# Optimization experiments

Hardware: AMD Instinct MI355X
Metric: run time of the kernel (lower is better)

The kernel has to match this reference:

```python
import jax, jax.numpy as jnp
import numpy as np

D_MODEL = 1024
D_CODEX = 64
CODEX_SIZE = 8192
BETA = 1.0
EPS_NORM = 1e-12
EPS_LN = 1e-5


def l2norm(x):
    # F.normalize(p=2, dim=-1, eps=1e-12): x / max(||x||, eps)
    n = jnp.sqrt(jnp.sum(x * x, axis=-1, keepdims=True))
    return x / jnp.maximum(n, EPS_NORM)


def setup_inputs() -> dict:
    key = jax.random.key(0)
    ks = jax.random.split(key, 8)
    B, S = 4, 2048
    Z = jax.random.normal(ks[0], (B, S, D_MODEL), dtype=jnp.float32)
    W1 = 0.02 * jax.random.normal(ks[1], (D_MODEL, D_MODEL), dtype=jnp.float32)
    b1 = jnp.zeros((D_MODEL,), dtype=jnp.float32)
    W2 = 0.02 * jax.random.normal(ks[2], (D_MODEL, D_CODEX), dtype=jnp.float32)
    b2 = jnp.zeros((D_CODEX,), dtype=jnp.float32)
    codex = l2norm(jax.random.normal(ks[3], (CODEX_SIZE, D_CODEX), dtype=jnp.float32))
    ln_w = jnp.ones((D_CODEX,), dtype=jnp.float32)
    ln_b = jnp.zeros((D_CODEX,), dtype=jnp.float32)
    Wp = 0.02 * jax.random.normal(ks[4], (D_CODEX, D_MODEL), dtype=jnp.float32)
    bp = jnp.zeros((D_MODEL,), dtype=jnp.float32)
    return {"Z": Z, "W1": W1, "b1": b1, "W2": W2, "b2": b2,
            "codex": codex, "ln_w": ln_w, "ln_b": ln_b, "Wp": Wp, "bp": bp}


def reference(Z, W1, b1, W2, b2, codex, ln_w, ln_b, Wp, bp):
    # pre_proj: Linear -> Tanh -> Linear, then l2-normalize into codex space
    Z_e = jnp.tanh(Z @ W1 + b1) @ W2 + b2            # (B, S, d_codex)
    Z_e = l2norm(Z_e)
    flat = Z_e.reshape(-1, D_CODEX)                  # (N, d_codex)
    # squared-L2 distances: |z|^2 + |c|^2 - 2 z.c
    dists = (jnp.sum(flat * flat, axis=-1, keepdims=True)
             + jnp.sum(codex * codex, axis=-1)[None, :]
             - 2.0 * jnp.einsum('nd,cd->nc', flat, codex))  # (N, K)
    idxs = jnp.argmin(dists, axis=-1).reshape(Z_e.shape[:-1])  # (B, S)
    codex_probs = jax.nn.one_hot(idxs, CODEX_SIZE, dtype=Z_e.dtype)  # (B, S, K)
    Z_q = codex[idxs]                                 # (B, S, d_codex)
    # commitment loss (codex is an EMA buffer, no gradient through it)
    loss = BETA * jnp.mean((jax.lax.stop_gradient(Z_q) - Z_e) ** 2)
    # straight-through estimator
    Z_q = Z_e + jax.lax.stop_gradient(Z_q - Z_e)
    # layernorm over d_codex
    mu = jnp.mean(Z_q, axis=-1, keepdims=True)
    var = jnp.mean((Z_q - mu) ** 2, axis=-1, keepdims=True)
    Z_q = (Z_q - mu) * jax.lax.rsqrt(var + EPS_LN) * ln_w + ln_b
    # post_proj back to d_model
    Z_q = Z_q @ Wp + bp                               # (B, S, d_model)
    return Z_q, loss, codex_probs
```

## Files before the change

### kernel.cpp

```cpp
#include <hip/hip_runtime.h>
#include <math.h>
#include <stdint.h>

#define N_TOK   8192
#define DMODEL  1024
#define DCODEX  64
#define KCODES  8192

__global__ __launch_bounds__(256) void codenorm_kernel(const float* __restrict__ codex,
                                                       float* __restrict__ cn2) {
    int k = blockIdx.x * 256 + threadIdx.x;
    const float4* p = (const float4*)(codex + (size_t)k * DCODEX);
    float s = 0.f;
#pragma unroll
    for (int i = 0; i < 16; ++i) {
        float4 v = p[i];
        s += v.x * v.x + v.y * v.y + v.z * v.z + v.w * v.w;
    }
    cn2[k] = s;
}

__global__ __launch_bounds__(256, 2) void gemm1_tanh_kernel(const float* __restrict__ Z,
                                                            const float* __restrict__ W1,
                                                            const float* __restrict__ b1,
                                                            float* __restrict__ H) {
    __shared__ float As[16][132];
    __shared__ float Bs[16][260];
    const int tid = threadIdx.x;
    const int row0 = blockIdx.x * 128;
    const int col0 = blockIdx.y * 256;
    const int ty = tid >> 5;
    const int tx = tid & 31;

    float acc[16][8];
#pragma unroll
    for (int i = 0; i < 16; ++i)
#pragma unroll
        for (int j = 0; j < 8; ++j) acc[i][j] = 0.f;

    for (int k0 = 0; k0 < DMODEL; k0 += 16) {
#pragma unroll
        for (int t = 0; t < 2; ++t) {
            int q = tid + t * 256;
            int r = q >> 2;
            int kc = (q & 3) * 4;
            float4 v = *(const float4*)(Z + (size_t)(row0 + r) * DMODEL + k0 + kc);
            As[kc + 0][r] = v.x; As[kc + 1][r] = v.y;
            As[kc + 2][r] = v.z; As[kc + 3][r] = v.w;
        }
#pragma unroll
        for (int t = 0; t < 4; ++t) {
            int q = tid + t * 256;
            int kk = q >> 6;
            int c4 = (q & 63) * 4;
            *(float4*)&Bs[kk][c4] =
                *(const float4*)(W1 + (size_t)(k0 + kk) * DMODEL + col0 + c4);
        }
        __syncthreads();
#pragma unroll
        for (int k = 0; k < 16; ++k) {
            float a[16], b[8];
            *(float4*)&a[0]  = *(const float4*)&As[k][ty * 16 + 0];
            *(float4*)&a[4]  = *(const float4*)&As[k][ty * 16 + 4];
            *(float4*)&a[8]  = *(const float4*)&As[k][ty * 16 + 8];
            *(float4*)&a[12] = *(const float4*)&As[k][ty * 16 + 12];
            *(float4*)&b[0]  = *(const float4*)&Bs[k][tx * 8 + 0];
            *(float4*)&b[4]  = *(const float4*)&Bs[k][tx * 8 + 4];
#pragma unroll
            for (int i = 0; i < 16; ++i)
#pragma unroll
                for (int j = 0; j < 8; ++j)
                    acc[i][j] = fmaf(a[i], b[j], acc[i][j]);
        }
        __syncthreads();
    }
    float bv[8];
    *(float4*)&bv[0] = *(const float4*)(b1 + col0 + tx * 8);
    *(float4*)&bv[4] = *(const float4*)(b1 + col0 + tx * 8 + 4);
#pragma unroll
    for (int i = 0; i < 16; ++i) {
        float o[8];
#pragma unroll
        for (int j = 0; j < 8; ++j) o[j] = tanhf(acc[i][j] + bv[j]);
        size_t off = (size_t)(row0 + ty * 16 + i) * DMODEL + col0 + tx * 8;
        *(float4*)(H + off)     = *(float4*)&o[0];
        *(float4*)(H + off + 4) = *(float4*)&o[4];
    }
}

__global__ __launch_bounds__(256) void gemm2_norm_kernel(const float* __restrict__ H,
                                                         const float* __restrict__ W2,
                                                         const float* __restrict__ b2,
                                                         float* __restrict__ Ze) {
    __shared__ float As[32][68];
    __shared__ float Bs[32][68];
    const int tid = threadIdx.x;
    const int row0 = blockIdx.x * 64;
    const int ty = tid >> 4, tx = tid & 15;

    float acc[4][4];
#pragma unroll
    for (int i = 0; i < 4; ++i)
#pragma unroll
        for (int j = 0; j < 4; ++j) acc[i][j] = 0.f;

    for (int k0 = 0; k0 < DMODEL; k0 += 32) {
#pragma unroll
        for (int t = 0; t < 2; ++t) {
            int q = tid + t * 256;
            int r = q >> 3;
            int k4 = (q & 7) * 4;
            float4 v = *(const float4*)(H + (size_t)(row0 + r) * DMODEL + k0 + k4);
            As[k4 + 0][r] = v.x; As[k4 + 1][r] = v.y;
            As[k4 + 2][r] = v.z; As[k4 + 3][r] = v.w;
        }
#pragma unroll
        for (int t = 0; t < 2; ++t) {
            int q = tid + t * 256;
            int kk = q >> 4;
            int c4 = (q & 15) * 4;
            *(float4*)&Bs[kk][c4] = *(const float4*)(W2 + (size_t)(k0 + kk) * DCODEX + c4);
        }
        __syncthreads();
#pragma unroll
        for (int k = 0; k < 32; ++k) {
            float4 a = *(const float4*)&As[k][ty * 4];
            float4 b = *(const float4*)&Bs[k][tx * 4];
            float av[4] = {a.x, a.y, a.z, a.w};
            float bw[4] = {b.x, b.y, b.z, b.w};
#pragma unroll
            for (int i = 0; i < 4; ++i)
#pragma unroll
                for (int j = 0; j < 4; ++j)
                    acc[i][j] = fmaf(av[i], bw[j], acc[i][j]);
        }
        __syncthreads();
    }
    float4 b2v4 = *(const float4*)(b2 + tx * 4);
    float b2v[4] = {b2v4.x, b2v4.y, b2v4.z, b2v4.w};
#pragma unroll
    for (int i = 0; i < 4; ++i) {
        float e[4];
#pragma unroll
        for (int j = 0; j < 4; ++j) e[j] = acc[i][j] + b2v[j];
        float ss = e[0] * e[0] + e[1] * e[1] + e[2] * e[2] + e[3] * e[3];
        ss += __shfl_xor(ss, 8, 64);
        ss += __shfl_xor(ss, 4, 64);
        ss += __shfl_xor(ss, 2, 64);
        ss += __shfl_xor(ss, 1, 64);
        float nrm = fmaxf(sqrtf(ss), 1e-12f);
        float o[4];
#pragma unroll
        for (int j = 0; j < 4; ++j) o[j] = e[j] / nrm;
        *(float4*)(Ze + (size_t)(row0 + ty * 4 + i) * DCODEX + tx * 4) = *(float4*)&o[0];
    }
}

__device__ __forceinline__ unsigned fenc(float f) {
    unsigned u = __float_as_uint(f);
    return (u & 0x80000000u) ? ~u : (u | 0x80000000u);
}

__global__ __launch_bounds__(256) void dist_argmin_kernel(const float* __restrict__ Ze,
                                                          const float* __restrict__ codex,
                                                          const float* __restrict__ cn2,
                                                          unsigned long long* __restrict__ gbest) {
    __shared__ float Zs[64][132];
    __shared__ float Cs[32][132];
    __shared__ unsigned long long red[128];
    const int tid = threadIdx.x;
    const int row0 = blockIdx.x * 128;
    const int strip0 = blockIdx.y * 1024;
    const int ty = tid >> 4, tx = tid & 15;

    if (tid < 128) red[tid] = 0xFFFFFFFFFFFFFFFFull;
#pragma unroll
    for (int t = 0; t < 8; ++t) {
        int q = tid + t * 256;
        int r = q >> 4;
        int d4 = (q & 15) * 4;
        float4 v = *(const float4*)(Ze + (size_t)(row0 + r) * DCODEX + d4);
        Zs[d4 + 0][r] = v.x; Zs[d4 + 1][r] = v.y;
        Zs[d4 + 2][r] = v.z; Zs[d4 + 3][r] = v.w;
    }

    float bv[8];
    int bi[8];
#pragma unroll
    for (int i = 0; i < 8; ++i) { bv[i] = INFINITY; bi[i] = 0; }

    for (int c0 = 0; c0 < 1024; c0 += 128) {
        const int cbase = strip0 + c0;
        float cn[8];
        *(float4*)&cn[0] = *(const float4*)(cn2 + cbase + tx * 8);
        *(float4*)&cn[4] = *(const float4*)(cn2 + cbase + tx * 8 + 4);
        float s[8][8];
#pragma unroll
        for (int i = 0; i < 8; ++i)
#pragma unroll
            for (int j = 0; j < 8; ++j) s[i][j] = 0.f;

        for (int h = 0; h < 2; ++h) {
            __syncthreads();
#pragma unroll
            for (int t = 0; t < 4; ++t) {
                int q = tid + t * 256;
                int c = q >> 3;
                int d4 = (q & 7) * 4;
                float4 v = *(const float4*)(codex + (size_t)(cbase + c) * DCODEX + h * 32 + d4);
                Cs[d4 + 0][c] = v.x; Cs[d4 + 1][c] = v.y;
                Cs[d4 + 2][c] = v.z; Cs[d4 + 3][c] = v.w;
            }
            __syncthreads();
#pragma unroll
            for (int d = 0; d < 32; ++d) {
                float a[8], b[8];
                *(float4*)&a[0] = *(const float4*)&Zs[h * 32 + d][ty * 8];
                *(float4*)&a[4] = *(const float4*)&Zs[h * 32 + d][ty * 8 + 4];
                *(float4*)&b[0] = *(const float4*)&Cs[d][tx * 8];
                *(float4*)&b[4] = *(const float4*)&Cs[d][tx * 8 + 4];
#pragma unroll
                for (int i = 0; i < 8; ++i)
#pragma unroll
                    for (int j = 0; j < 8; ++j)
                        s[i][j] = fmaf(a[i], b[j], s[i][j]);
            }
        }
#pragma unroll
        for (int i = 0; i < 8; ++i)
#pragma unroll
            for (int j = 0; j < 8; ++j) {
                float dist = fmaf(-2.0f, s[i][j], cn[j]);
                if (dist < bv[i]) { bv[i] = dist; bi[i] = cbase + tx * 8 + j; }
            }
    }
#pragma unroll
    for (int i = 0; i < 8; ++i) {
        unsigned long long key =
            ((unsigned long long)fenc(bv[i]) << 32) | (unsigned)bi[i];
        atomicMin(&red[ty * 8 + i], key);
    }
    __syncthreads();
    if (tid < 128) atomicMin(&gbest[row0 + tid], red[tid]);
}

__global__ __launch_bounds__(256) void scatter_onehot_kernel(const unsigned long long* __restrict__ gbest,
                                                             int* __restrict__ idxbuf,
                                                             float* __restrict__ probs) {
    int n = blockIdx.x * 256 + threadIdx.x;
    unsigned id = (unsigned)(gbest[n] & 0xFFFFFFFFull);
    idxbuf[n] = (int)id;
    probs[(size_t)n * KCODES + id] = 1.0f;
}

__global__ __launch_bounds__(256) void ln_gemm3_loss_kernel(const int* __restrict__ idxbuf,
                                                            const float* __restrict__ codex,
                                                            const float* __restrict__ Ze,
                                                            const float* __restrict__ ln_w,
                                                            const float* __restrict__ ln_b,
                                                            const float* __restrict__ Wp,
                                                            const float* __restrict__ bp,
                                                            float* __restrict__ Zq,
                                                            float* __restrict__ loss) {
    __shared__ float A[16][64];
    __shared__ float lossAcc;
    const int tid = threadIdx.x;
    const int row0 = blockIdx.x * 16;
    if (tid == 0) lossAcc = 0.f;
    __syncthreads();
    const int w = tid >> 6, l = tid & 63;
    const float lw = ln_w[l], lb = ln_b[l];
    float lsum = 0.f;
#pragma unroll
    for (int g = 0; g < 4; ++g) {
        int r = w * 4 + g;
        int row = row0 + r;
        int id = idxbuf[row];
        float zq = codex[(size_t)id * DCODEX + l];
        float ze = Ze[(size_t)row * DCODEX + l];
        float dlt = zq - ze;
        float val = ze + dlt;
        float s = val;
#pragma unroll
        for (int m = 32; m >= 1; m >>= 1) s += __shfl_xor(s, m, 64);
        float mu = s * 0.015625f;
        float c = val - mu;
        float v2 = c * c;
#pragma unroll
        for (int m = 32; m >= 1; m >>= 1) v2 += __shfl_xor(v2, m, 64);
        float var = v2 * 0.015625f;
        float y = c * (1.0f / sqrtf(var + 1e-5f)) * lw + lb;
        A[r][l] = y;
        float d2 = dlt * dlt;
#pragma unroll
        for (int m = 32; m >= 1; m >>= 1) d2 += __shfl_xor(d2, m, 64);
        if (l == 0) lsum += d2;
    }
    if (l == 0) atomicAdd(&lossAcc, lsum);
    __syncthreads();
    if (tid == 0) atomicAdd(loss, lossAcc * (1.0f / 524288.0f));

#pragma unroll 1
    for (int jj = 0; jj < 4; ++jj) {
        int j = jj * 256 + tid;
        float wp[64];
#pragma unroll
        for (int d = 0; d < 64; ++d) wp[d] = Wp[(size_t)d * DMODEL + j];
        float bias = bp[j];
#pragma unroll 1
        for (int n = 0; n < 16; ++n) {
            float acc = bias;
#pragma unroll
            for (int d4 = 0; d4 < 16; ++d4) {
                float4 av = *(const float4*)&A[n][d4 * 4];
                acc = fmaf(av.x, wp[d4 * 4 + 0], acc);
                acc = fmaf(av.y, wp[d4 * 4 + 1], acc);
                acc = fmaf(av.z, wp[d4 * 4 + 2], acc);
                acc = fmaf(av.w, wp[d4 * 4 + 3], acc);
            }
            Zq[(size_t)(row0 + n) * DMODEL + j] = acc;
        }
    }
}

extern "C" void kernel_launch(void* const* d_in, const int* in_sizes, int n_in,
                              void* d_out, int out_size, void* d_ws, size_t ws_size,
                              hipStream_t stream) {
    const float* Z     = (const float*)d_in[0];
    const float* W1    = (const float*)d_in[1];
    const float* b1    = (const float*)d_in[2];
    const float* W2    = (const float*)d_in[3];
    const float* b2    = (const float*)d_in[4];
    const float* codex = (const float*)d_in[5];
    const float* ln_w  = (const float*)d_in[6];
    const float* ln_b  = (const float*)d_in[7];
    const float* Wp    = (const float*)d_in[8];
    const float* bp    = (const float*)d_in[9];

    float* out      = (float*)d_out;
    float* Zq_out   = out;
    float* loss_out = out + (size_t)N_TOK * DMODEL;
    float* probs    = loss_out + 1;

    char* ws = (char*)d_ws;
    float* H   = (float*)ws;
    float* Ze  = H + (size_t)N_TOK * DMODEL;
    float* cn2 = Ze + (size_t)N_TOK * DCODEX;
    unsigned long long* gbest = (unsigned long long*)(cn2 + KCODES);
    int* idxbuf = (int*)(gbest + N_TOK);

    hipMemsetAsync(loss_out, 0, (size_t)(1 + (size_t)N_TOK * KCODES) * sizeof(float), stream);
    hipMemsetAsync(gbest, 0xFF, (size_t)N_TOK * sizeof(unsigned long long), stream);

    codenorm_kernel<<<KCODES / 256, 256, 0, stream>>>(codex, cn2);
    gemm1_tanh_kernel<<<dim3(N_TOK / 128, DMODEL / 256), 256, 0, stream>>>(Z, W1, b1, H);
    gemm2_norm_kernel<<<N_TOK / 64, 256, 0, stream>>>(H, W2, b2, Ze);
    dist_argmin_kernel<<<dim3(N_TOK / 128, KCODES / 1024), 256, 0, stream>>>(Ze, codex, cn2, gbest);
    scatter_onehot_kernel<<<N_TOK / 256, 256, 0, stream>>>(gbest, idxbuf, probs);
    ln_gemm3_loss_kernel<<<N_TOK / 16, 256, 0, stream>>>(idxbuf, codex, Ze, ln_w, ln_b,
                                                         Wp, bp, Zq_out, loss_out);
}
```

Measured before the change: 800.0 us.

## Retile GEMMs, double-buffer gemm1, split LN and post-projection into tiled GEMM

The first GEMM moves to 128x128 tiles with an 8x8 per-thread microtile, register-prefetched double-buffered shared memory, and strided fragment indexing to cut LDS bank conflicts. The second GEMM uses smaller row blocks for more parallelism. The distance kernel uses the same strided column and row mapping. The fused LN+post-projection kernel is split into a per-row LN/loss kernel and a shared-memory tiled GEMM that reuses the H buffer for its input. This trades a grid-wide loss atomic per row and an extra launch for much better reuse in the post-projection.

```diff
diff --git a/kernel.cpp b/kernel.cpp
--- a/kernel.cpp
+++ b/kernel.cpp
@@ -24,122 +24,139 @@
                                                             const float* __restrict__ W1,
                                                             const float* __restrict__ b1,
                                                             float* __restrict__ H) {
-    __shared__ float As[16][132];
-    __shared__ float Bs[16][260];
+    __shared__ float As[2][16][132];
+    __shared__ float Bs[2][16][132];
     const int tid = threadIdx.x;
     const int row0 = blockIdx.x * 128;
-    const int col0 = blockIdx.y * 256;
-    const int ty = tid >> 5;
-    const int tx = tid & 31;
-
-    float acc[16][8];
-#pragma unroll
-    for (int i = 0; i < 16; ++i)
+    const int col0 = blockIdx.y * 128;
+    const int ty = tid >> 4, tx = tid & 15;
+
+    float acc[8][8];
+#pragma unroll
+    for (int i = 0; i < 8; ++i)
 #pragma unroll
         for (int j = 0; j < 8; ++j) acc[i][j] = 0.f;
 
+    float4 pa[2], pb[2];
+#pragma unroll
+    for (int t = 0; t < 2; ++t) {
+        int q = tid + t * 256;
+        pa[t] = *(const float4*)(Z + (size_t)(row0 + (q >> 2)) * DMODEL + ((q & 3) * 4));
+        pb[t] = *(const float4*)(W1 + (size_t)(q >> 5) * DMODEL + col0 + (q & 31) * 4);
+    }
+#pragma unroll
+    for (int t = 0; t < 2; ++t) {
+        int q = tid + t * 256;
+        int r = q >> 2, kc = (q & 3) * 4;
+        As[0][kc + 0][r] = pa[t].x; As[0][kc + 1][r] = pa[t].y;
+        As[0][kc + 2][r] = pa[t].z; As[0][kc + 3][r] = pa[t].w;
+        *(float4*)&Bs[0][q >> 5][(q & 31) * 4] = pb[t];
+    }
+    __syncthreads();
+
+    int buf = 0;
     for (int k0 = 0; k0 < DMODEL; k0 += 16) {
-#pragma unroll
-        for (int t = 0; t < 2; ++t) {
-            int q = tid + t * 256;
-            int r = q >> 2;
-            int kc = (q & 3) * 4;
-            float4 v = *(const float4*)(Z + (size_t)(row0 + r) * DMODEL + k0 + kc);
-            As[kc + 0][r] = v.x; As[kc + 1][r] = v.y;
-            As[kc + 2][r] = v.z; As[kc + 3][r] = v.w;
-        }
-#pragma unroll
-        for (int t = 0; t < 4; ++t) {
-            int q = tid + t * 256;
-            int kk = q >> 6;
-            int c4 = (q & 63) * 4;
-            *(float4*)&Bs[kk][c4] =
-                *(const float4*)(W1 + (size_t)(k0 + kk) * DMODEL + col0 + c4);
-        }
-        __syncthreads();
+        const bool more = (k0 + 16) < DMODEL;
+        if (more) {
+#pragma unroll
+            for (int t = 0; t < 2; ++t) {
+                int q = tid + t * 256;
+                pa[t] = *(const float4*)(Z + (size_t)(row0 + (q >> 2)) * DMODEL + k0 + 16 + ((q & 3) * 4));
+                pb[t] = *(const float4*)(W1 + (size_t)(k0 + 16 + (q >> 5)) * DMODEL + col0 + (q & 31) * 4);
+            }
+        }
 #pragma unroll
         for (int k = 0; k < 16; ++k) {
-            float a[16], b[8];
-            *(float4*)&a[0]  = *(const float4*)&As[k][ty * 16 + 0];
-            *(float4*)&a[4]  = *(const float4*)&As[k][ty * 16 + 4];
-            *(float4*)&a[8]  = *(const float4*)&As[k][ty * 16 + 8];
-            *(float4*)&a[12] = *(const float4*)&As[k][ty * 16 + 12];
-            *(float4*)&b[0]  = *(const float4*)&Bs[k][tx * 8 + 0];
-            *(float4*)&b[4]  = *(const float4*)&Bs[k][tx * 8 + 4];
-#pragma unroll
-            for (int i = 0; i < 16; ++i)
+            float a[8], b[8];
+            *(float4*)&a[0] = *(const float4*)&As[buf][k][ty * 4];
+            *(float4*)&a[4] = *(const float4*)&As[buf][k][64 + ty * 4];
+            *(float4*)&b[0] = *(const float4*)&Bs[buf][k][tx * 4];
+            *(float4*)&b[4] = *(const float4*)&Bs[buf][k][64 + tx * 4];
+#pragma unroll
+            for (int i = 0; i < 8; ++i)
 #pragma unroll
                 for (int j = 0; j < 8; ++j)
                     acc[i][j] = fmaf(a[i], b[j], acc[i][j]);
         }
+        if (more) {
+#pragma unroll
+            for (int t = 0; t < 2; ++t) {
+                int q = tid + t * 256;
+                int r = q >> 2, kc = (q & 3) * 4;
+                As[buf ^ 1][kc + 0][r] = pa[t].x; As[buf ^ 1][kc + 1][r] = pa[t].y;
+                As[buf ^ 1][kc + 2][r] = pa[t].z; As[buf ^ 1][kc + 3][r] = pa[t].w;
+                *(float4*)&Bs[buf ^ 1][q >> 5][(q & 31) * 4] = pb[t];
+            }
+        }
         __syncthreads();
-    }
+        buf ^= 1;
+    }
+
     float bv[8];
-    *(float4*)&bv[0] = *(const float4*)(b1 + col0 + tx * 8);
-    *(float4*)&bv[4] = *(const float4*)(b1 + col0 + tx * 8 + 4);
-#pragma unroll
-    for (int i = 0; i < 16; ++i) {
-        float o[8];
-#pragma unroll
-        for (int j = 0; j < 8; ++j) o[j] = tanhf(acc[i][j] + bv[j]);
-        size_t off = (size_t)(row0 + ty * 16 + i) * DMODEL + col0 + tx * 8;
-        *(float4*)(H + off)     = *(float4*)&o[0];
-        *(float4*)(H + off + 4) = *(float4*)&o[4];
-    }
+    *(float4*)&bv[0] = *(const float4*)(b1 + col0 + tx * 4);
+    *(float4*)&bv[4] = *(const float4*)(b1 + col0 + 64 + tx * 4);
+#pragma unroll
+    for (int half = 0; half < 2; ++half)
+#pragma unroll
+        for (int i = 0; i < 4; ++i) {
+            int r = row0 + half * 64 + ty * 4 + i;
+            float o[8];
+#pragma unroll
+            for (int j = 0; j < 8; ++j) o[j] = tanhf(acc[half * 4 + i][j] + bv[j]);
+            *(float4*)(H + (size_t)r * DMODEL + col0 + tx * 4)      = *(float4*)&o[0];
+            *(float4*)(H + (size_t)r * DMODEL + col0 + 64 + tx * 4) = *(float4*)&o[4];
+        }
 }
 
 __global__ __launch_bounds__(256) void gemm2_norm_kernel(const float* __restrict__ H,
                                                          const float* __restrict__ W2,
                                                          const float* __restrict__ b2,
                                                          float* __restrict__ Ze) {
-    __shared__ float As[32][68];
-    __shared__ float Bs[32][68];
+    __shared__ float As[64][36];
+    __shared__ float Bs[64][68];
     const int tid = threadIdx.x;
-    const int row0 = blockIdx.x * 64;
+    const int row0 = blockIdx.x * 32;
     const int ty = tid >> 4, tx = tid & 15;
 
-    float acc[4][4];
-#pragma unroll
-    for (int i = 0; i < 4; ++i)
+    float acc[2][4];
+#pragma unroll
+    for (int i = 0; i < 2; ++i)
 #pragma unroll
         for (int j = 0; j < 4; ++j) acc[i][j] = 0.f;
 
-    for (int k0 = 0; k0 < DMODEL; k0 += 32) {
+    for (int k0 = 0; k0 < DMODEL; k0 += 64) {
+        __syncthreads();
 #pragma unroll
         for (int t = 0; t < 2; ++t) {
             int q = tid + t * 256;
-            int r = q >> 3;
-            int k4 = (q & 7) * 4;
+            int r = q >> 4, k4 = (q & 15) * 4;
             float4 v = *(const float4*)(H + (size_t)(row0 + r) * DMODEL + k0 + k4);
             As[k4 + 0][r] = v.x; As[k4 + 1][r] = v.y;
             As[k4 + 2][r] = v.z; As[k4 + 3][r] = v.w;
         }
 #pragma unroll
-        for (int t = 0; t < 2; ++t) {
+        for (int t = 0; t < 4; ++t) {
             int q = tid + t * 256;
-            int kk = q >> 4;
-            int c4 = (q & 15) * 4;
+            int kk = q >> 4, c4 = (q & 15) * 4;
             *(float4*)&Bs[kk][c4] = *(const float4*)(W2 + (size_t)(k0 + kk) * DCODEX + c4);
         }
         __syncthreads();
 #pragma unroll
-        for (int k = 0; k < 32; ++k) {
-            float4 a = *(const float4*)&As[k][ty * 4];
+        for (int k = 0; k < 64; ++k) {
+            float2 a = *(const float2*)&As[k][ty * 2];
             float4 b = *(const float4*)&Bs[k][tx * 4];
-            float av[4] = {a.x, a.y, a.z, a.w};
             float bw[4] = {b.x, b.y, b.z, b.w};
 #pragma unroll
-            for (int i = 0; i < 4; ++i)
-#pragma unroll
-                for (int j = 0; j < 4; ++j)
-                    acc[i][j] = fmaf(av[i], bw[j], acc[i][j]);
-        }
-        __syncthreads();
+            for (int j = 0; j < 4; ++j) {
+                acc[0][j] = fmaf(a.x, bw[j], acc[0][j]);
+                acc[1][j] = fmaf(a.y, bw[j], acc[1][j]);
+            }
+        }
     }
     float4 b2v4 = *(const float4*)(b2 + tx * 4);
     float b2v[4] = {b2v4.x, b2v4.y, b2v4.z, b2v4.w};
 #pragma unroll
-    for (int i = 0; i < 4; ++i) {
+    for (int i = 0; i < 2; ++i) {
         float e[4];
 #pragma unroll
         for (int j = 0; j < 4; ++j) e[j] = acc[i][j] + b2v[j];
@@ -152,7 +169,7 @@
         float o[4];
 #pragma unroll
         for (int j = 0; j < 4; ++j) o[j] = e[j] / nrm;
-        *(float4*)(Ze + (size_t)(row0 + ty * 4 + i) * DCODEX + tx * 4) = *(float4*)&o[0];
+        *(float4*)(Ze + (size_t)(row0 + ty * 2 + i) * DCODEX + tx * 4) = *(float4*)&o[0];
     }
 }
 
@@ -177,8 +194,7 @@
 #pragma unroll
     for (int t = 0; t < 8; ++t) {
         int q = tid + t * 256;
-        int r = q >> 4;
-        int d4 = (q & 15) * 4;
+        int r = q >> 4, d4 = (q & 15) * 4;
         float4 v = *(const float4*)(Ze + (size_t)(row0 + r) * DCODEX + d4);
         Zs[d4 + 0][r] = v.x; Zs[d4 + 1][r] = v.y;
         Zs[d4 + 2][r] = v.z; Zs[d4 + 3][r] = v.w;
@@ -192,8 +208,8 @@
     for (int c0 = 0; c0 < 1024; c0 += 128) {
         const int cbase = strip0 + c0;
         float cn[8];
-        *(float4*)&cn[0] = *(const float4*)(cn2 + cbase + tx * 8);
-        *(float4*)&cn[4] = *(const float4*)(cn2 + cbase + tx * 8 + 4);
+        *(float4*)&cn[0] = *(const float4*)(cn2 + cbase + tx * 4);
+        *(float4*)&cn[4] = *(const float4*)(cn2 + cbase + 64 + tx * 4);
         float s[8][8];
 #pragma unroll
         for (int i = 0; i < 8; ++i)
@@ -205,8 +221,7 @@
 #pragma unroll
             for (int t = 0; t < 4; ++t) {
                 int q = tid + t * 256;
-                int c = q >> 3;
-                int d4 = (q & 7) * 4;
+                int c = q >> 3, d4 = (q & 7) * 4;
                 float4 v = *(const float4*)(codex + (size_t)(cbase + c) * DCODEX + h * 32 + d4);
                 Cs[d4 + 0][c] = v.x; Cs[d4 + 1][c] = v.y;
                 Cs[d4 + 2][c] = v.z; Cs[d4 + 3][c] = v.w;
@@ -215,10 +230,10 @@
 #pragma unroll
             for (int d = 0; d < 32; ++d) {
                 float a[8], b[8];
-                *(float4*)&a[0] = *(const float4*)&Zs[h * 32 + d][ty * 8];
-                *(float4*)&a[4] = *(const float4*)&Zs[h * 32 + d][ty * 8 + 4];
-                *(float4*)&b[0] = *(const float4*)&Cs[d][tx * 8];
-                *(float4*)&b[4] = *(const float4*)&Cs[d][tx * 8 + 4];
+                *(float4*)&a[0] = *(const float4*)&Zs[h * 32 + d][ty * 4];
+                *(float4*)&a[4] = *(const float4*)&Zs[h * 32 + d][64 + ty * 4];
+                *(float4*)&b[0] = *(const float4*)&Cs[d][tx * 4];
+                *(float4*)&b[4] = *(const float4*)&Cs[d][64 + tx * 4];
 #pragma unroll
                 for (int i = 0; i < 8; ++i)
 #pragma unroll
@@ -231,14 +246,16 @@
 #pragma unroll
             for (int j = 0; j < 8; ++j) {
                 float dist = fmaf(-2.0f, s[i][j], cn[j]);
-                if (dist < bv[i]) { bv[i] = dist; bi[i] = cbase + tx * 8 + j; }
+                int col = cbase + ((j < 4) ? (tx * 4 + j) : (64 + tx * 4 + j - 4));
+                if (dist < bv[i]) { bv[i] = dist; bi[i] = col; }
             }
     }
 #pragma unroll
     for (int i = 0; i < 8; ++i) {
+        int li = (i < 4) ? (ty * 4 + i) : (64 + ty * 4 + i - 4);
         unsigned long long key =
             ((unsigned long long)fenc(bv[i]) << 32) | (unsigned)bi[i];
-        atomicMin(&red[ty * 8 + i], key);
+        atomicMin(&red[li], key);
     }
     __syncthreads();
     if (tid < 128) atomicMin(&gbest[row0 + tid], red[tid]);
@@ -253,74 +270,95 @@
     probs[(size_t)n * KCODES + id] = 1.0f;
 }
 
-__global__ __launch_bounds__(256) void ln_gemm3_loss_kernel(const int* __restrict__ idxbuf,
-                                                            const float* __restrict__ codex,
-                                                            const float* __restrict__ Ze,
-                                                            const float* __restrict__ ln_w,
-                                                            const float* __restrict__ ln_b,
-                                                            const float* __restrict__ Wp,
-                                                            const float* __restrict__ bp,
-                                                            float* __restrict__ Zq,
-                                                            float* __restrict__ loss) {
-    __shared__ float A[16][64];
-    __shared__ float lossAcc;
+__global__ __launch_bounds__(256) void ln_loss_kernel(const int* __restrict__ idxbuf,
+                                                      const float* __restrict__ codex,
+                                                      const float* __restrict__ Ze,
+                                                      const float* __restrict__ ln_w,
+                                                      const float* __restrict__ ln_b,
+                                                      float* __restrict__ Aln,
+                                                      float* __restrict__ loss) {
     const int tid = threadIdx.x;
-    const int row0 = blockIdx.x * 16;
-    if (tid == 0) lossAcc = 0.f;
+    const int w = tid >> 6, l = tid & 63;
+    const int row = blockIdx.x * 4 + w;
+    int id = idxbuf[row];
+    float zq = codex[(size_t)id * DCODEX + l];
+    float ze = Ze[(size_t)row * DCODEX + l];
+    float dlt = zq - ze;
+    float val = ze + dlt;
+    float s = val;
+#pragma unroll
+    for (int m = 32; m >= 1; m >>= 1) s += __shfl_xor(s, m, 64);
+    float mu = s * 0.015625f;
+    float c = val - mu;
+    float v2 = c * c;
+#pragma unroll
+    for (int m = 32; m >= 1; m >>= 1) v2 += __shfl_xor(v2, m, 64);
+    float var = v2 * 0.015625f;
+    float y = c * (1.0f / sqrtf(var + 1e-5f)) * ln_w[l] + ln_b[l];
+    Aln[(size_t)row * DCODEX + l] = y;
+    float d2 = dlt * dlt;
+#pragma unroll
+    for (int m = 32; m >= 1; m >>= 1) d2 += __shfl_xor(d2, m, 64);
+    if (l == 0) atomicAdd(loss, d2 * (1.0f / 524288.0f));
+}
+
+__global__ __launch_bounds__(256) void gemm3_kernel(const float* __restrict__ Aln,
+                                                    const float* __restrict__ Wp,
+                                                    const float* __restrict__ bp,
+                                                    float* __restrict__ Zq) {
+    __shared__ float As[64][132];
+    __shared__ float Bs[64][68];
+    const int tid = threadIdx.x;
+    const int row0 = blockIdx.x * 128;
+    const int col0 = blockIdx.y * 64;
+    const int ty = tid >> 4, tx = tid & 15;
+
+#pragma unroll
+    for (int t = 0; t < 8; ++t) {
+        int q = tid + t * 256;
+        int r = q >> 4, d4 = (q & 15) * 4;
+        float4 v = *(const float4*)(Aln + (size_t)(row0 + r) * DCODEX + d4);
+        As[d4 + 0][r] = v.x; As[d4 + 1][r] = v.y;
+        As[d4 + 2][r] = v.z; As[d4 + 3][r] = v.w;
+    }
+#pragma unroll
+    for (int t = 0; t < 4; ++t) {
+        int q = tid + t * 256;
+        int kk = q >> 4, c4 = (q & 15) * 4;
+        *(float4*)&Bs[kk][c4] = *(const float4*)(Wp + (size_t)kk * DMODEL + col0 + c4);
+    }
     __syncthreads();
-    const int w = tid >> 6, l = tid & 63;
-    const float lw = ln_w[l], lb = ln_b[l];
-    float lsum = 0.f;
-#pragma unroll
-    for (int g = 0; g < 4; ++g) {
-        int r = w * 4 + g;
-        int row = row0 + r;
-        int id = idxbuf[row];
-        float zq = codex[(size_t)id * DCODEX + l];
-        float ze = Ze[(size_t)row * DCODEX + l];
-        float dlt = zq - ze;
-        float val = ze + dlt;
-        float s = val;
-#pragma unroll
-        for (int m = 32; m >= 1; m >>= 1) s += __shfl_xor(s, m, 64);
-        float mu = s * 0.015625f;
-        float c = val - mu;
-        float v2 = c * c;
-#pragma unroll
-        for (int m = 32; m >= 1; m >>= 1) v2 += __shfl_xor(v2, m, 64);
-        float var = v2 * 0.015625f;
-        float y = c * (1.0f / sqrtf(var + 1e-5f)) * lw + lb;
-        A[r][l] = y;
-        float d2 = dlt * dlt;
-#pragma unroll
-        for (int m = 32; m >= 1; m >>= 1) d2 += __shfl_xor(d2, m, 64);
-        if (l == 0) lsum += d2;
-    }
-    if (l == 0) atomicAdd(&lossAcc, lsum);
-    __syncthreads();
-    if (tid == 0) atomicAdd(loss, lossAcc * (1.0f / 524288.0f));
-
-#pragma unroll 1
-    for (int jj = 0; jj < 4; ++jj) {
-        int j = jj * 256 + tid;
-        float wp[64];
-#pragma unroll
-        for (int d = 0; d < 64; ++d) wp[d] = Wp[(size_t)d * DMODEL + j];
-        float bias = bp[j];
-#pragma unroll 1
-        for (int n = 0; n < 16; ++n) {
-            float acc = bias;
-#pragma unroll
-            for (int d4 = 0; d4 < 16; ++d4) {
-                float4 av = *(const float4*)&A[n][d4 * 4];
-                acc = fmaf(av.x, wp[d4 * 4 + 0], acc);
-                acc = fmaf(av.y, wp[d4 * 4 + 1], acc);
-                acc = fmaf(av.z, wp[d4 * 4 + 2], acc);
-                acc = fmaf(av.w, wp[d4 * 4 + 3], acc);
-            }
-            Zq[(size_t)(row0 + n) * DMODEL + j] = acc;
-        }
-    }
+
+    float acc[8][4];
+#pragma unroll
+    for (int i = 0; i < 8; ++i)
+#pragma unroll
+        for (int j = 0; j < 4; ++j) acc[i][j] = 0.f;
+#pragma unroll
+    for (int k = 0; k < 64; ++k) {
+        float a[8];
+        *(float4*)&a[0] = *(const float4*)&As[k][ty * 4];
+        *(float4*)&a[4] = *(const float4*)&As[k][64 + ty * 4];
+        float4 b = *(const float4*)&Bs[k][tx * 4];
+        float bw[4] = {b.x, b.y, b.z, b.w};
+#pragma unroll
+        for (int i = 0; i < 8; ++i)
+#pragma unroll
+            for (int j = 0; j < 4; ++j)
+                acc[i][j] = fmaf(a[i], bw[j], acc[i][j]);
+    }
+    float4 bp4 = *(const float4*)(bp + col0 + tx * 4);
+    float bb[4] = {bp4.x, bp4.y, bp4.z, bp4.w};
+#pragma unroll
+    for (int half = 0; half < 2; ++half)
+#pragma unroll
+        for (int i = 0; i < 4; ++i) {
+            int r = row0 + half * 64 + ty * 4 + i;
+            float o[4];
+#pragma unroll
+            for (int j = 0; j < 4; ++j) o[j] = acc[half * 4 + i][j] + bb[j];
+            *(float4*)(Zq + (size_t)r * DMODEL + col0 + tx * 4) = *(float4*)&o[0];
+        }
 }
 
 extern "C" void kernel_launch(void* const* d_in, const int* in_sizes, int n_in,
@@ -344,6 +382,7 @@
 
     char* ws = (char*)d_ws;
     float* H   = (float*)ws;
+    float* Aln = H;
     float* Ze  = H + (size_t)N_TOK * DMODEL;
     float* cn2 = Ze + (size_t)N_TOK * DCODEX;
     unsigned long long* gbest = (unsigned long long*)(cn2 + KCODES);
@@ -353,10 +392,10 @@
     hipMemsetAsync(gbest, 0xFF, (size_t)N_TOK * sizeof(unsigned long long), stream);
 
     codenorm_kernel<<<KCODES / 256, 256, 0, stream>>>(codex, cn2);
-    gemm1_tanh_kernel<<<dim3(N_TOK / 128, DMODEL / 256), 256, 0, stream>>>(Z, W1, b1, H);
-    gemm2_norm_kernel<<<N_TOK / 64, 256, 0, stream>>>(H, W2, b2, Ze);
+    gemm1_tanh_kernel<<<dim3(N_TOK / 128, DMODEL / 128), 256, 0, stream>>>(Z, W1, b1, H);
+    gemm2_norm_kernel<<<N_TOK / 32, 256, 0, stream>>>(H, W2, b2, Ze);
     dist_argmin_kernel<<<dim3(N_TOK / 128, KCODES / 1024), 256, 0, stream>>>(Ze, codex, cn2, gbest);
     scatter_onehot_kernel<<<N_TOK / 256, 256, 0, stream>>>(gbest, idxbuf, probs);
-    ln_gemm3_loss_kernel<<<N_TOK / 16, 256, 0, stream>>>(idxbuf, codex, Ze, ln_w, ln_b,
-                                                         Wp, bp, Zq_out, loss_out);
-}
+    ln_loss_kernel<<<N_TOK / 4, 256, 0, stream>>>(idxbuf, codex, Ze, ln_w, ln_b, Aln, loss_out);
+    gemm3_kernel<<<dim3(N_TOK / 128, DMODEL / 64), 256, 0, stream>>>(Aln, Wp, bp, Zq_out);
+}
```

Result: slower. 1.803 ms (+125.4%).
